# Optimization experiments

Hardware: AMD Instinct MI355X
Metric: run time of the kernel (lower is better)

## Reference

```python
import jax, jax.numpy as jnp
import numpy as np

N_NODES = 50000
NEG_SLOPE = 0.2  # PyG GATConv default
EPS = 1e-16      # PyG softmax denominator epsilon


def _gat_conv(x, edge_index, W, att_src, att_dst, bias):
    """Single-head PyG-style GATConv with self-loops.
    x: [N, F_in], edge_index: [2, E] (row 0 = src/j, row 1 = dst/i).
    """
    n = x.shape[0]
    loop = jnp.arange(n, dtype=edge_index.dtype)
    src = jnp.concatenate([edge_index[0], loop])  # [E+N]
    dst = jnp.concatenate([edge_index[1], loop])  # [E+N]

    h = x @ W                                      # [N, F_out]
    a_src = h @ att_src                            # [N]
    a_dst = h @ att_dst                            # [N]

    e = jax.nn.leaky_relu(a_src[src] + a_dst[dst], NEG_SLOPE)  # [E+N]
    # segment softmax over incoming edges of each dst node
    m = jax.ops.segment_max(e, dst, num_segments=n)
    m = jnp.where(jnp.isfinite(m), m, 0.0)
    e = jnp.exp(e - m[dst])
    s = jax.ops.segment_sum(e, dst, num_segments=n)
    alpha = e / (s[dst] + EPS)                     # [E+N]

    out = jax.ops.segment_sum(alpha[:, None] * h[src], dst, num_segments=n)
    return out + bias


def setup_inputs() -> dict:
    key = jax.random.key(0)
    ks = jax.random.split(key, 10)
    d_in, d_hid, d_emb = 128, 64, 64
    n_edges = 800000
    x = jax.random.normal(ks[0], (N_NODES, d_in), dtype=jnp.float32)
    edge_index = jax.random.randint(ks[1], (2, n_edges), 0, N_NODES, dtype=jnp.int64)
    def glorot(k, shape):
        lim = float(np.sqrt(6.0 / sum(shape)))
        return jax.random.uniform(k, shape, jnp.float32, -lim, lim)
    return {
        "x": x,
        "edge_index": edge_index,
        "W1": glorot(ks[2], (d_in, d_hid)),
        "att_src1": glorot(ks[3], (d_hid,)),
        "att_dst1": glorot(ks[4], (d_hid,)),
        "b1": jnp.zeros((d_hid,), jnp.float32),
        "W2": glorot(ks[5], (d_hid, d_emb)),
        "att_src2": glorot(ks[6], (d_emb,)),
        "att_dst2": glorot(ks[7], (d_emb,)),
        "b2": jnp.zeros((d_emb,), jnp.float32),
    }


def reference(x, edge_index, W1, att_src1, att_dst1, b1, W2, att_src2, att_dst2, b2):
    x1 = jax.nn.relu(_gat_conv(x, edge_index, W1, att_src1, att_dst1, b1))
    # dropout is identity in eval mode
    x2 = _gat_conv(x1, edge_index, W2, att_src2, att_dst2, b2)
    return x2
```

## Files before the change

### kernel.cpp

```cpp
#include <hip/hip_runtime.h>
#include <hip/hip_bf16.h>

#define F_OUT 64
#define NEG_SLOPE 0.2f
#define SOFT_EPS 1e-16f
#define BW 256
#define CH 8192
#define TH 512
#define TH3 512

typedef short short8 __attribute__((ext_vector_type(8)));
typedef float floatx4 __attribute__((ext_vector_type(4)));
typedef unsigned short ushort4v __attribute__((ext_vector_type(4)));
typedef unsigned short ushort8v __attribute__((ext_vector_type(8)));

__device__ __forceinline__ unsigned short f2bf_bits(float v) {
    __hip_bfloat16 hb = __float2bfloat16(v);
    return *(unsigned short*)&hb;
}
__device__ __forceinline__ float bf_bits2f(unsigned short u) {
    __hip_bfloat16 hb = *(__hip_bfloat16*)&u;
    return __bfloat162float(hb);
}
__device__ __forceinline__ float read_any(const void* src, int off, int bf) {
    return bf ? __bfloat162float(((const __hip_bfloat16*)src)[off])
              : ((const float*)src)[off];
}
__device__ __forceinline__ int get_idx(const void* ei, int i64, long long pos) {
    return i64 ? (int)((const long long*)ei)[pos] : ((const int*)ei)[pos];
}

__device__ __forceinline__ void detect_local(const unsigned* wbits, const unsigned* ebits,
                                             int* sm_bf, int* sm_i64) {
    if (threadIdx.x < 64) {
        unsigned w = wbits[threadIdx.x];
        unsigned e = (w >> 7) & 0xFFu;
        unsigned long long mb = __ballot(e >= 0x60u && e <= 0x7Eu);
        unsigned long long mz = __ballot(ebits[2 * threadIdx.x + 1] == 0u);
        if (threadIdx.x == 0) { *sm_bf = (__popcll(mb) > 32); *sm_i64 = (__popcll(mz) > 32); }
    }
    __syncthreads();
}

__global__ void count_prep(const void* __restrict__ ei, int* __restrict__ table,
                           const void* w1, const void* as1, const void* ad1, const void* b1,
                           const void* w2, const void* as2, const void* ad2, const void* b2,
                           unsigned short* __restrict__ wt1, unsigned short* __restrict__ wt2,
                           float* __restrict__ vecs, int* __restrict__ flags,
                           int E, int total, int NB, int nchunks, int n1, int n2, int K1) {
    __shared__ int cnt[1024];
    __shared__ int s_bf, s_i64;
    detect_local((const unsigned*)w1, (const unsigned*)ei, &s_bf, &s_i64);
    int bf = s_bf, i64 = s_i64;
    int g = blockIdx.x, tid = threadIdx.x;
    if (g == 0 && tid == 0) { flags[0] = bf; flags[1] = i64; }

    if (g < nchunks) {
        for (int k = tid; k < NB; k += TH) cnt[k] = 0;
        __syncthreads();
        int base = g * CH;
        int lim = base + CH < total ? base + CH : total;
        for (int t = base + tid; t < lim; t += TH) {
            int i = t < E ? get_idx(ei, i64, (long long)E + t) : t - E;
            atomicAdd(&cnt[i >> 8], 1);
        }
        __syncthreads();
        for (int k = tid; k < NB; k += TH) table[k * nchunks + g] = cnt[k];
    } else {
        int wtotal = n1 + n2 + 384;
        for (int t = tid; t < wtotal; t += TH) {
            if (t < n1) {
                int n = t / K1, k = t - n * K1;
                wt1[t] = f2bf_bits(read_any(w1, k * F_OUT + n, bf));
            } else if (t < n1 + n2) {
                int u = t - n1;
                int n = u >> 6, k = u & 63;
                wt2[u] = f2bf_bits(read_any(w2, k * F_OUT + n, bf));
            } else {
                int u = t - n1 - n2;
                const void* srcp[6] = {as1, ad1, b1, as2, ad2, b2};
                vecs[u] = read_any(srcp[u >> 6], u & 63, bf);
            }
        }
    }
}

template <int K, int WAVES>
__device__ __forceinline__ void gemm_body(int blk, int tid,
                          const void* __restrict__ xv, const unsigned short* __restrict__ Wt,
                          const float* __restrict__ att_s, const float* __restrict__ att_d,
                          unsigned short* __restrict__ h, float* __restrict__ a_s,
                          float* __restrict__ a_d, int N, int bf) {
    int lane = tid & 63;
    int m0 = (blk * WAVES + (tid >> 6)) * 16;
    if (m0 >= N) return;
    int c = lane & 15, quad = lane >> 4;
    int arow = m0 + c;
    if (arow >= N) arow = N - 1;

    floatx4 acc0 = {0.f, 0.f, 0.f, 0.f};
    floatx4 acc1 = acc0, acc2 = acc0, acc3 = acc0;

    for (int kc = 0; kc < K; kc += 32) {
        int ka = kc + quad * 8;
        short8 a;
        if (bf) {
            a = *(const short8*)((const unsigned short*)xv + (size_t)arow * K + ka);
        } else {
            const float* xp = (const float*)xv + (size_t)arow * K + ka;
#pragma unroll
            for (int j = 0; j < 8; ++j) a[j] = (short)f2bf_bits(xp[j]);
        }
        short8 b0 = *(const short8*)(Wt + (size_t)(c)      * K + ka);
        short8 b1 = *(const short8*)(Wt + (size_t)(16 + c) * K + ka);
        short8 b2 = *(const short8*)(Wt + (size_t)(32 + c) * K + ka);
        short8 b3 = *(const short8*)(Wt + (size_t)(48 + c) * K + ka);
        acc0 = __builtin_amdgcn_mfma_f32_16x16x32_bf16(a, b0, acc0, 0, 0, 0);
        acc1 = __builtin_amdgcn_mfma_f32_16x16x32_bf16(a, b1, acc1, 0, 0, 0);
        acc2 = __builtin_amdgcn_mfma_f32_16x16x32_bf16(a, b2, acc2, 0, 0, 0);
        acc3 = __builtin_amdgcn_mfma_f32_16x16x32_bf16(a, b3, acc3, 0, 0, 0);
    }

    float as0 = att_s[c],      as1 = att_s[16 + c], as2 = att_s[32 + c], as3 = att_s[48 + c];
    float ad0 = att_d[c],      ad1 = att_d[16 + c], ad2 = att_d[32 + c], ad3 = att_d[48 + c];
#pragma unroll
    for (int reg = 0; reg < 4; ++reg) {
        int row = m0 + quad * 4 + reg;
        float vs = acc0[reg] * as0 + acc1[reg] * as1 + acc2[reg] * as2 + acc3[reg] * as3;
        float vd = acc0[reg] * ad0 + acc1[reg] * ad1 + acc2[reg] * ad2 + acc3[reg] * ad3;
#pragma unroll
        for (int off = 1; off < 16; off <<= 1) {
            vs += __shfl_xor(vs, off);
            vd += __shfl_xor(vd, off);
        }
        if (row < N) {
            if (c == 0) { a_s[row] = vs; a_d[row] = vd; }
            unsigned short* hr = h + (size_t)row * F_OUT + c;
            hr[0]  = f2bf_bits(acc0[reg]);
            hr[16] = f2bf_bits(acc1[reg]);
            hr[32] = f2bf_bits(acc2[reg]);
            hr[48] = f2bf_bits(acc3[reg]);
        }
    }
}

__global__ void __launch_bounds__(TH)
scatter_gemm1(const void* __restrict__ ei, const int* __restrict__ table,
              unsigned* __restrict__ staged, int* __restrict__ segbeg,
              int* __restrict__ row_ptr, const void* __restrict__ xv,
              const unsigned short* __restrict__ Wt,
              const float* __restrict__ att_s, const float* __restrict__ att_d,
              unsigned short* __restrict__ h, float* __restrict__ a_s,
              float* __restrict__ a_d, const unsigned* __restrict__ wbits,
              int E, int total, int NB, int nchunks, int N) {
    __shared__ int s_bf, s_i64;
    detect_local(wbits, (const unsigned*)ei, &s_bf, &s_i64);
    int tid = threadIdx.x;
    if ((int)blockIdx.x >= nchunks) {
        gemm_body<128, 8>(blockIdx.x - nchunks, tid, xv, Wt, att_s, att_d,
                          h, a_s, a_d, N, s_bf);
        return;
    }
    __shared__ int s_scan[TH];
    __shared__ int s_cur[1024];
    int g = blockIdx.x;
    int i64 = s_i64;
    int b0 = 0;
    if (tid < NB) {
        const int* row = table + (size_t)tid * nchunks;
        int rsum = 0, rpart = 0;
        for (int c2 = 0; c2 < nchunks; ++c2) {
            int v = row[c2];
            rsum += v;
            rpart += (c2 < g) ? v : 0;
        }
        b0 = rsum;
        s_cur[tid] = rpart;
    }
    s_scan[tid] = (tid < NB) ? b0 : 0;
    __syncthreads();
    for (int off = 1; off < TH; off <<= 1) {
        int v = (tid >= off) ? s_scan[tid - off] : 0;
        __syncthreads();
        s_scan[tid] += v;
        __syncthreads();
    }
    if (tid < NB) {
        int excl = s_scan[tid] - b0;
        s_cur[tid] = excl + s_cur[tid];
        if (g == 0) segbeg[tid] = excl;
    }
    if (g == 0 && tid == 0) { segbeg[NB] = total; row_ptr[N] = total; }
    __syncthreads();
    int base = g * CH;
    int lim = base + CH < total ? base + CH : total;
    for (int t = base + tid; t < lim; t += TH) {
        int i = t < E ? get_idx(ei, i64, (long long)E + t) : t - E;
        int j = t < E ? get_idx(ei, i64, t) : t - E;
        int pos = atomicAdd(&s_cur[i >> 8], 1);
        staged[pos] = ((unsigned)(i & 255) << 24) | (unsigned)j;
    }
}

__global__ void __launch_bounds__(TH3)
bucket_csr(const unsigned* __restrict__ staged, const int* __restrict__ segbeg,
           int* __restrict__ row_ptr, int* __restrict__ eidx, int N) {
    __shared__ int ldeg[BW];
    __shared__ int lcur[BW];
    __shared__ int wtot[4];
    int b = blockIdx.x;
    int t = threadIdx.x;
    int seg_beg = segbeg[b];
    int seg_end = segbeg[b + 1];
    if (t < BW) ldeg[t] = 0;
    __syncthreads();
    for (int p = seg_beg + t; p < seg_end; p += TH3)
        atomicAdd(&ldeg[staged[p] >> 24], 1);
    __syncthreads();
    int lane = t & 63, w = t >> 6;
    int d = 0, v = 0;
    if (t < BW) {
        d = ldeg[t];
        v = d;
#pragma unroll
        for (int off = 1; off < 64; off <<= 1) {
            int u = __shfl_up(v, off);
            if (lane >= off) v += u;
        }
        if (lane == 63) wtot[w] = v;
    }
    __syncthreads();
    if (t < BW) {
        int woff = 0;
        for (int k = 0; k < w; ++k) woff += wtot[k];
        int excl = v - d + woff;
        int node = b * BW + t;
        if (node < N) row_ptr[node] = seg_beg + excl;
        lcur[t] = excl;
    }
    __syncthreads();
    for (int p = seg_beg + t; p < seg_end; p += TH3) {
        unsigned pk = staged[p];
        int pos = atomicAdd(&lcur[pk >> 24], 1);
        eidx[seg_beg + pos] = (int)(pk & 0xFFFFFFu);
    }
}

__device__ __forceinline__ void gather_node8(int i, int grp, int c8,
                                             const int* __restrict__ row_ptr,
                                             const int* __restrict__ eidx,
                                             const float* __restrict__ a_s,
                                             const float* __restrict__ a_d,
                                             const unsigned short* __restrict__ h,
                                             float* se_out, float acc[8]) {
    int beg = row_ptr[i];
    int end = row_ptr[i + 1];
    int len = end - beg;
    float ad = a_d[i];
    int gb = beg + ((len * grp) >> 3);
    int ge = beg + ((len * (grp + 1)) >> 3);
    float se = 0.f;
#pragma unroll
    for (int k = 0; k < 8; ++k) acc[k] = 0.f;

    int p = gb;
    for (; p + 1 < ge; p += 2) {
        int j0 = eidx[p];
        int j1 = eidx[p + 1];
        ushort8v hv0 = *(const ushort8v*)(h + (((size_t)j0) << 6) + (c8 << 3));
        ushort8v hv1 = *(const ushort8v*)(h + (((size_t)j1) << 6) + (c8 << 3));
        float e0 = a_s[j0] + ad;
        float e1 = a_s[j1] + ad;
        float w0 = __expf(fmaxf(e0, NEG_SLOPE * e0));
        float w1 = __expf(fmaxf(e1, NEG_SLOPE * e1));
        se += w0 + w1;
#pragma unroll
        for (int k = 0; k < 8; ++k)
            acc[k] += w0 * bf_bits2f(hv0[k]) + w1 * bf_bits2f(hv1[k]);
    }
    if (p < ge) {
        int j0 = eidx[p];
        ushort8v hv0 = *(const ushort8v*)(h + (((size_t)j0) << 6) + (c8 << 3));
        float e0 = a_s[j0] + ad;
        float w0 = __expf(fmaxf(e0, NEG_SLOPE * e0));
        se += w0;
#pragma unroll
        for (int k = 0; k < 8; ++k) acc[k] += w0 * bf_bits2f(hv0[k]);
    }

#pragma unroll
    for (int off = 8; off < 64; off <<= 1) {
        se += __shfl_xor(se, off);
#pragma unroll
        for (int k = 0; k < 8; ++k) acc[k] += __shfl_xor(acc[k], off);
    }
    *se_out = se;
}

#define XST 72
__global__ void __launch_bounds__(1024)
gather1_gemm2(const int* __restrict__ row_ptr, const int* __restrict__ eidx,
              const float* __restrict__ a_s, const float* __restrict__ a_d,
              const unsigned short* __restrict__ h, const float* __restrict__ bias,
              const unsigned short* __restrict__ Wt2,
              const float* __restrict__ att_s2, const float* __restrict__ att_d2,
              unsigned short* __restrict__ h2, float* __restrict__ a_s2,
              float* __restrict__ a_d2, int N) {
    __shared__ unsigned short x1t[16 * XST];
    int tid = threadIdx.x;
    int lane = tid & 63;
    int wv = tid >> 6;
    int grp = lane >> 3, c8 = lane & 7;
    int i = blockIdx.x * 16 + wv;

    if (i < N) {
        float se, acc[8];
        gather_node8(i, grp, c8, row_ptr, eidx, a_s, a_d, h, &se, acc);
        if (grp == 0) {
            int col = c8 << 3;
            float inv = 1.f / (se + SOFT_EPS);
            ushort8v ov;
#pragma unroll
            for (int k = 0; k < 8; ++k) {
                float v = acc[k] * inv + bias[col + k];
                ov[k] = f2bf_bits(v > 0.f ? v : 0.f);
            }
            *(ushort8v*)(x1t + wv * XST + col) = ov;
        }
    } else if (grp == 0) {
        *(ushort8v*)(x1t + wv * XST + (c8 << 3)) = (ushort8v){0, 0, 0, 0, 0, 0, 0, 0};
    }
    __syncthreads();

    if (wv == 0) {
        int quad = lane >> 4, c = lane & 15;
        int m0 = blockIdx.x * 16;
        floatx4 acc0 = {0.f, 0.f, 0.f, 0.f};
        floatx4 acc1 = acc0, acc2 = acc0, acc3 = acc0;
#pragma unroll
        for (int kc = 0; kc < 64; kc += 32) {
            int ka = kc + quad * 8;
            short8 a = *(const short8*)(x1t + c * XST + ka);
            short8 b0 = *(const short8*)(Wt2 + (size_t)(c)      * 64 + ka);
            short8 b1 = *(const short8*)(Wt2 + (size_t)(16 + c) * 64 + ka);
            short8 b2 = *(const short8*)(Wt2 + (size_t)(32 + c) * 64 + ka);
            short8 b3 = *(const short8*)(Wt2 + (size_t)(48 + c) * 64 + ka);
            acc0 = __builtin_amdgcn_mfma_f32_16x16x32_bf16(a, b0, acc0, 0, 0, 0);
            acc1 = __builtin_amdgcn_mfma_f32_16x16x32_bf16(a, b1, acc1, 0, 0, 0);
            acc2 = __builtin_amdgcn_mfma_f32_16x16x32_bf16(a, b2, acc2, 0, 0, 0);
            acc3 = __builtin_amdgcn_mfma_f32_16x16x32_bf16(a, b3, acc3, 0, 0, 0);
        }
        float as0 = att_s2[c],      as1 = att_s2[16 + c], as2 = att_s2[32 + c], as3 = att_s2[48 + c];
        float ad0 = att_d2[c],      ad1 = att_d2[16 + c], ad2 = att_d2[32 + c], ad3 = att_d2[48 + c];
#pragma unroll
        for (int reg = 0; reg < 4; ++reg) {
            int row = m0 + quad * 4 + reg;
            float vs = acc0[reg] * as0 + acc1[reg] * as1 + acc2[reg] * as2 + acc3[reg] * as3;
            float vd = acc0[reg] * ad0 + acc1[reg] * ad1 + acc2[reg] * ad2 + acc3[reg] * ad3;
#pragma unroll
            for (int off = 1; off < 16; off <<= 1) {
                vs += __shfl_xor(vs, off);
                vd += __shfl_xor(vd, off);
            }
            if (row < N) {
                if (c == 0) { a_s2[row] = vs; a_d2[row] = vd; }
                unsigned short* hr = h2 + (size_t)row * F_OUT + c;
                hr[0]  = f2bf_bits(acc0[reg]);
                hr[16] = f2bf_bits(acc1[reg]);
                hr[32] = f2bf_bits(acc2[reg]);
                hr[48] = f2bf_bits(acc3[reg]);
            }
        }
    }
}

__global__ void __launch_bounds__(256)
node_gather_out(const int* __restrict__ row_ptr, const int* __restrict__ eidx,
                const float* __restrict__ a_s, const float* __restrict__ a_d,
                const unsigned short* __restrict__ h, const float* __restrict__ bias,
                void* __restrict__ out, int N, const int* __restrict__ flags) {
    int lane = threadIdx.x & 63;
    int i = blockIdx.x * 4 + (threadIdx.x >> 6);
    if (i >= N) return;
    int grp = lane >> 3, c8 = lane & 7;
    float se, acc[8];
    gather_node8(i, grp, c8, row_ptr, eidx, a_s, a_d, h, &se, acc);
    if (grp == 0) {
        int col = c8 << 3;
        float inv = 1.f / (se + SOFT_EPS);
        float v[8];
#pragma unroll
        for (int k = 0; k < 8; ++k) v[k] = acc[k] * inv + bias[col + k];
        size_t o = (size_t)i * F_OUT + col;
        if (flags[0]) {
            ushort8v ov;
#pragma unroll
            for (int k = 0; k < 8; ++k) ov[k] = f2bf_bits(v[k]);
            *(ushort8v*)((unsigned short*)out + o) = ov;
        } else {
            floatx4 o0 = {v[0], v[1], v[2], v[3]};
            floatx4 o1 = {v[4], v[5], v[6], v[7]};
            *(floatx4*)((float*)out + o) = o0;
            *(floatx4*)((float*)out + o + 4) = o1;
        }
    }
}

extern "C" void kernel_launch(void* const* d_in, const int* in_sizes, int n_in,
                              void* d_out, int out_size, void* d_ws, size_t ws_size,
                              hipStream_t stream) {
    const void* x   = d_in[0];
    const void* ei  = d_in[1];
    const void* W1  = d_in[2];
    const void* as1 = d_in[3];
    const void* ad1 = d_in[4];
    const void* b1  = d_in[5];
    const void* W2  = d_in[6];
    const void* as2 = d_in[7];
    const void* ad2 = d_in[8];
    const void* b2  = d_in[9];

    int E  = in_sizes[1] / 2;
    int n1 = in_sizes[2];
    int n2 = in_sizes[6];
    int K1 = n1 / F_OUT;
    int N  = in_sizes[0] / K1;
    int total = E + N;
    int NB = (N + BW - 1) / BW;
    int nchunks = (total + CH - 1) / CH;
    int M = NB * nchunks;

    size_t nf = (size_t)N * F_OUT;
    char* wsb = (char*)d_ws;
    unsigned short* h   = (unsigned short*)wsb;
    unsigned short* h2  = h + nf;
    unsigned short* wt1 = h2 + nf;
    unsigned short* wt2 = wt1 + n1;
    float* a_s  = (float*)(wt2 + n2 + ((n1 + n2) & 1));
    float* a_d  = a_s + N;
    float* a_s2 = a_d + N;
    float* a_d2 = a_s2 + N;
    float* vecs = a_d2 + N;
    float* cAs1 = vecs,       *cAd1 = vecs + 64,  *cB1 = vecs + 128;
    float* cAs2 = vecs + 192, *cAd2 = vecs + 256, *cB2 = vecs + 320;
    int* flags    = (int*)(vecs + 384);
    int* row_ptr  = flags + 8;
    int* eidx     = row_ptr + N + 1;
    unsigned* staged = (unsigned*)(eidx + total);
    int* table    = (int*)(staged + total);
    int* segbeg   = table + M;

    int blkG1 = (N + 127) / 128;
    int blkFuse = (N + 15) / 16;
    int blkNode = (N + 3) / 4;

    count_prep<<<nchunks + 1, TH, 0, stream>>>(ei, table, W1, as1, ad1, b1,
                                               W2, as2, ad2, b2, wt1, wt2, vecs, flags,
                                               E, total, NB, nchunks, n1, n2, K1);
    scatter_gemm1<<<nchunks + blkG1, TH, 0, stream>>>(ei, table, staged, segbeg, row_ptr,
                                                      x, wt1, cAs1, cAd1, h, a_s, a_d,
                                                      (const unsigned*)W1,
                                                      E, total, NB, nchunks, N);
    bucket_csr<<<NB, TH3, 0, stream>>>(staged, segbeg, row_ptr, eidx, N);
    gather1_gemm2<<<blkFuse, 1024, 0, stream>>>(row_ptr, eidx, a_s, a_d, h, cB1,
                                                wt2, cAs2, cAd2, h2, a_s2, a_d2, N);
    node_gather_out<<<blkNode, 256, 0, stream>>>(row_ptr, eidx, a_s2, a_d2, h2, cB2,
                                                 d_out, N, flags);
}
```

Measured before the change: 188.7 us.

## Fold layer-2 attention vectors into W2 and split layer-2 GEMM across four waves

```diff
diff --git a/kernel.cpp b/kernel.cpp
--- a/kernel.cpp
+++ b/kernel.cpp
@@ -11,7 +11,6 @@
 
 typedef short short8 __attribute__((ext_vector_type(8)));
 typedef float floatx4 __attribute__((ext_vector_type(4)));
-typedef unsigned short ushort4v __attribute__((ext_vector_type(4)));
 typedef unsigned short ushort8v __attribute__((ext_vector_type(8)));
 
 __device__ __forceinline__ unsigned short f2bf_bits(float v) {
@@ -46,7 +45,8 @@
                            const void* w1, const void* as1, const void* ad1, const void* b1,
                            const void* w2, const void* as2, const void* ad2, const void* b2,
                            unsigned short* __restrict__ wt1, unsigned short* __restrict__ wt2,
-                           float* __restrict__ vecs, int* __restrict__ flags,
+                           float* __restrict__ vecs, float* __restrict__ waS2,
+                           float* __restrict__ waD2, int* __restrict__ flags,
                            int E, int total, int NB, int nchunks, int n1, int n2, int K1) {
     __shared__ int cnt[1024];
     __shared__ int s_bf, s_i64;
@@ -82,6 +82,14 @@
                 vecs[u] = read_any(srcp[u >> 6], u & 63, bf);
             }
         }
+        for (int t = tid; t < 128; t += TH) {
+            int k = t & 63;
+            const void* av = (t < 64) ? as2 : ad2;
+            float s = 0.f;
+            for (int n = 0; n < 64; ++n)
+                s += read_any(w2, k * 64 + n, bf) * read_any(av, n, bf);
+            (t < 64 ? waS2 : waD2)[k] = s;
+        }
     }
 }
 
@@ -108,8 +116,13 @@
             a = *(const short8*)((const unsigned short*)xv + (size_t)arow * K + ka);
         } else {
             const float* xp = (const float*)xv + (size_t)arow * K + ka;
-#pragma unroll
-            for (int j = 0; j < 8; ++j) a[j] = (short)f2bf_bits(xp[j]);
+            floatx4 f0 = *(const floatx4*)xp;
+            floatx4 f1 = *(const floatx4*)(xp + 4);
+#pragma unroll
+            for (int j = 0; j < 4; ++j) {
+                a[j]     = (short)f2bf_bits(f0[j]);
+                a[4 + j] = (short)f2bf_bits(f1[j]);
+            }
         }
         short8 b0 = *(const short8*)(Wt + (size_t)(c)      * K + ka);
         short8 b1 = *(const short8*)(Wt + (size_t)(16 + c) * K + ka);
@@ -298,12 +311,12 @@
 }
 
 #define XST 72
-__global__ void __launch_bounds__(1024)
+__global__ void __launch_bounds__(1024, 2)
 gather1_gemm2(const int* __restrict__ row_ptr, const int* __restrict__ eidx,
               const float* __restrict__ a_s, const float* __restrict__ a_d,
               const unsigned short* __restrict__ h, const float* __restrict__ bias,
               const unsigned short* __restrict__ Wt2,
-              const float* __restrict__ att_s2, const float* __restrict__ att_d2,
+              const float* __restrict__ waS2, const float* __restrict__ waD2,
               unsigned short* __restrict__ h2, float* __restrict__ a_s2,
               float* __restrict__ a_d2, int N) {
     __shared__ unsigned short x1t[16 * XST];
@@ -316,15 +329,34 @@
     if (i < N) {
         float se, acc[8];
         gather_node8(i, grp, c8, row_ptr, eidx, a_s, a_d, h, &se, acc);
+        int col = c8 << 3;
+        float inv = 1.f / (se + SOFT_EPS);
+        floatx4 ws0 = *(const floatx4*)(waS2 + col);
+        floatx4 ws1 = *(const floatx4*)(waS2 + col + 4);
+        floatx4 wd0 = *(const floatx4*)(waD2 + col);
+        floatx4 wd1 = *(const floatx4*)(waD2 + col + 4);
+        float v[8];
+        float ps = 0.f, pd = 0.f;
+#pragma unroll
+        for (int k = 0; k < 8; ++k) {
+            float x = acc[k] * inv + bias[col + k];
+            x = x > 0.f ? x : 0.f;
+            v[k] = x;
+            float fs = (k < 4) ? ws0[k] : ws1[k - 4];
+            float fd = (k < 4) ? wd0[k] : wd1[k - 4];
+            ps += x * fs;
+            pd += x * fd;
+        }
+#pragma unroll
+        for (int off = 1; off < 8; off <<= 1) {
+            ps += __shfl_xor(ps, off);
+            pd += __shfl_xor(pd, off);
+        }
+        if (lane == 0) { a_s2[i] = ps; a_d2[i] = pd; }
         if (grp == 0) {
-            int col = c8 << 3;
-            float inv = 1.f / (se + SOFT_EPS);
             ushort8v ov;
 #pragma unroll
-            for (int k = 0; k < 8; ++k) {
-                float v = acc[k] * inv + bias[col + k];
-                ov[k] = f2bf_bits(v > 0.f ? v : 0.f);
-            }
+            for (int k = 0; k < 8; ++k) ov[k] = f2bf_bits(v[k]);
             *(ushort8v*)(x1t + wv * XST + col) = ov;
         }
     } else if (grp == 0) {
@@ -332,49 +364,26 @@
     }
     __syncthreads();
 
-    if (wv == 0) {
+    if (wv < 4) {
         int quad = lane >> 4, c = lane & 15;
         int m0 = blockIdx.x * 16;
-        floatx4 acc0 = {0.f, 0.f, 0.f, 0.f};
-        floatx4 acc1 = acc0, acc2 = acc0, acc3 = acc0;
+        floatx4 g0 = {0.f, 0.f, 0.f, 0.f};
 #pragma unroll
         for (int kc = 0; kc < 64; kc += 32) {
             int ka = kc + quad * 8;
             short8 a = *(const short8*)(x1t + c * XST + ka);
-            short8 b0 = *(const short8*)(Wt2 + (size_t)(c)      * 64 + ka);
-            short8 b1 = *(const short8*)(Wt2 + (size_t)(16 + c) * 64 + ka);
-            short8 b2 = *(const short8*)(Wt2 + (size_t)(32 + c) * 64 + ka);
-            short8 b3 = *(const short8*)(Wt2 + (size_t)(48 + c) * 64 + ka);
-            acc0 = __builtin_amdgcn_mfma_f32_16x16x32_bf16(a, b0, acc0, 0, 0, 0);
-            acc1 = __builtin_amdgcn_mfma_f32_16x16x32_bf16(a, b1, acc1, 0, 0, 0);
-            acc2 = __builtin_amdgcn_mfma_f32_16x16x32_bf16(a, b2, acc2, 0, 0, 0);
-            acc3 = __builtin_amdgcn_mfma_f32_16x16x32_bf16(a, b3, acc3, 0, 0, 0);
-        }
-        float as0 = att_s2[c],      as1 = att_s2[16 + c], as2 = att_s2[32 + c], as3 = att_s2[48 + c];
-        float ad0 = att_d2[c],      ad1 = att_d2[16 + c], ad2 = att_d2[32 + c], ad3 = att_d2[48 + c];
+            short8 b = *(const short8*)(Wt2 + (size_t)(wv * 16 + c) * 64 + ka);
+            g0 = __builtin_amdgcn_mfma_f32_16x16x32_bf16(a, b, g0, 0, 0, 0);
+        }
 #pragma unroll
         for (int reg = 0; reg < 4; ++reg) {
             int row = m0 + quad * 4 + reg;
-            float vs = acc0[reg] * as0 + acc1[reg] * as1 + acc2[reg] * as2 + acc3[reg] * as3;
-            float vd = acc0[reg] * ad0 + acc1[reg] * ad1 + acc2[reg] * ad2 + acc3[reg] * ad3;
-#pragma unroll
-            for (int off = 1; off < 16; off <<= 1) {
-                vs += __shfl_xor(vs, off);
-                vd += __shfl_xor(vd, off);
-            }
-            if (row < N) {
-                if (c == 0) { a_s2[row] = vs; a_d2[row] = vd; }
-                unsigned short* hr = h2 + (size_t)row * F_OUT + c;
-                hr[0]  = f2bf_bits(acc0[reg]);
-                hr[16] = f2bf_bits(acc1[reg]);
-                hr[32] = f2bf_bits(acc2[reg]);
-                hr[48] = f2bf_bits(acc3[reg]);
-            }
-        }
-    }
-}
-
-__global__ void __launch_bounds__(256)
+            if (row < N) h2[(size_t)row * F_OUT + wv * 16 + c] = f2bf_bits(g0[reg]);
+        }
+    }
+}
+
+__global__ void __launch_bounds__(256, 8)
 node_gather_out(const int* __restrict__ row_ptr, const int* __restrict__ eidx,
                 const float* __restrict__ a_s, const float* __restrict__ a_d,
                 const unsigned short* __restrict__ h, const float* __restrict__ bias,
@@ -443,7 +452,9 @@
     float* vecs = a_d2 + N;
     float* cAs1 = vecs,       *cAd1 = vecs + 64,  *cB1 = vecs + 128;
     float* cAs2 = vecs + 192, *cAd2 = vecs + 256, *cB2 = vecs + 320;
-    int* flags    = (int*)(vecs + 384);
+    float* waS2 = vecs + 384;
+    float* waD2 = vecs + 448;
+    int* flags    = (int*)(vecs + 512);
     int* row_ptr  = flags + 8;
     int* eidx     = row_ptr + N + 1;
     unsigned* staged = (unsigned*)(eidx + total);
@@ -455,7 +466,8 @@
     int blkNode = (N + 3) / 4;
 
     count_prep<<<nchunks + 1, TH, 0, stream>>>(ei, table, W1, as1, ad1, b1,
-                                               W2, as2, ad2, b2, wt1, wt2, vecs, flags,
+                                               W2, as2, ad2, b2, wt1, wt2, vecs,
+                                               waS2, waD2, flags,
                                                E, total, NB, nchunks, n1, n2, K1);
     scatter_gemm1<<<nchunks + blkG1, TH, 0, stream>>>(ei, table, staged, segbeg, row_ptr,
                                                       x, wt1, cAs1, cAd1, h, a_s, a_d,
@@ -463,7 +475,7 @@
                                                       E, total, NB, nchunks, N);
     bucket_csr<<<NB, TH3, 0, stream>>>(staged, segbeg, row_ptr, eidx, N);
     gather1_gemm2<<<blkFuse, 1024, 0, stream>>>(row_ptr, eidx, a_s, a_d, h, cB1,
-                                                wt2, cAs2, cAd2, h2, a_s2, a_d2, N);
+                                                wt2, waS2, waD2, h2, a_s2, a_d2, N);
     node_gather_out<<<blkNode, 256, 0, stream>>>(row_ptr, eidx, a_s2, a_d2, h2, cB2,
                                                  d_out, N, flags);
 }
```

After: 192.9 us. 2.3% more time.

## Sort nodes by degree within buckets to balance fused gather-GEMM blocks

Applied to the files above, without the earlier changes.

```diff
diff --git a/kernel.cpp b/kernel.cpp
--- a/kernel.cpp
+++ b/kernel.cpp
@@ -5,13 +5,12 @@
 #define NEG_SLOPE 0.2f
 #define SOFT_EPS 1e-16f
 #define BW 256
-#define CH 8192
+#define CH 4096
 #define TH 512
-#define TH3 512
+#define TH3 1024
 
 typedef short short8 __attribute__((ext_vector_type(8)));
 typedef float floatx4 __attribute__((ext_vector_type(4)));
-typedef unsigned short ushort4v __attribute__((ext_vector_type(4)));
 typedef unsigned short ushort8v __attribute__((ext_vector_type(8)));
 
 __device__ __forceinline__ unsigned short f2bf_bits(float v) {
@@ -108,8 +107,13 @@
             a = *(const short8*)((const unsigned short*)xv + (size_t)arow * K + ka);
         } else {
             const float* xp = (const float*)xv + (size_t)arow * K + ka;
-#pragma unroll
-            for (int j = 0; j < 8; ++j) a[j] = (short)f2bf_bits(xp[j]);
+            floatx4 f0 = *(const floatx4*)xp;
+            floatx4 f1 = *(const floatx4*)(xp + 4);
+#pragma unroll
+            for (int j = 0; j < 4; ++j) {
+                a[j]     = (short)f2bf_bits(f0[j]);
+                a[4 + j] = (short)f2bf_bits(f1[j]);
+            }
         }
         short8 b0 = *(const short8*)(Wt + (size_t)(c)      * K + ka);
         short8 b1 = *(const short8*)(Wt + (size_t)(16 + c) * K + ka);
@@ -204,23 +208,29 @@
 
 __global__ void __launch_bounds__(TH3)
 bucket_csr(const unsigned* __restrict__ staged, const int* __restrict__ segbeg,
-           int* __restrict__ row_ptr, int* __restrict__ eidx, int N) {
+           int* __restrict__ row_ptr, int* __restrict__ eidx,
+           int* __restrict__ order, int N) {
     __shared__ int ldeg[BW];
     __shared__ int lcur[BW];
     __shared__ int wtot[4];
+    __shared__ int dcnt[128];
+    __shared__ int dcur[128];
     int b = blockIdx.x;
     int t = threadIdx.x;
     int seg_beg = segbeg[b];
     int seg_end = segbeg[b + 1];
     if (t < BW) ldeg[t] = 0;
+    if (t < 128) dcnt[t] = 0;
     __syncthreads();
     for (int p = seg_beg + t; p < seg_end; p += TH3)
         atomicAdd(&ldeg[staged[p] >> 24], 1);
     __syncthreads();
     int lane = t & 63, w = t >> 6;
-    int d = 0, v = 0;
+    int node = b * BW + t;
+    int d = 0, v = 0, dmin = 0;
     if (t < BW) {
         d = ldeg[t];
+        dmin = d < 127 ? d : 127;
         v = d;
 #pragma unroll
         for (int off = 1; off < 64; off <<= 1) {
@@ -234,11 +244,28 @@
         int woff = 0;
         for (int k = 0; k < w; ++k) woff += wtot[k];
         int excl = v - d + woff;
-        int node = b * BW + t;
-        if (node < N) row_ptr[node] = seg_beg + excl;
+        if (node < N) {
+            row_ptr[node] = seg_beg + excl;
+            atomicAdd(&dcnt[dmin], 1);
+        }
         lcur[t] = excl;
-    }
-    __syncthreads();
+        order[b * BW + t] = -1;
+    }
+    __syncthreads();
+    if (t < 128) dcur[t] = dcnt[t];
+    __syncthreads();
+    for (int off = 1; off < 128; off <<= 1) {
+        int u = (t < 128 && t >= off) ? dcnt[t - off] : 0;
+        __syncthreads();
+        if (t < 128) dcnt[t] += u;
+        __syncthreads();
+    }
+    if (t < 128) dcur[t] = dcnt[t] - dcur[t];
+    __syncthreads();
+    if (t < BW && node < N) {
+        int pos = atomicAdd(&dcur[dmin], 1);
+        order[b * BW + pos] = node;
+    }
     for (int p = seg_beg + t; p < seg_end; p += TH3) {
         unsigned pk = staged[p];
         int pos = atomicAdd(&lcur[pk >> 24], 1);
@@ -300,6 +327,7 @@
 #define XST 72
 __global__ void __launch_bounds__(1024)
 gather1_gemm2(const int* __restrict__ row_ptr, const int* __restrict__ eidx,
+              const int* __restrict__ order,
               const float* __restrict__ a_s, const float* __restrict__ a_d,
               const unsigned short* __restrict__ h, const float* __restrict__ bias,
               const unsigned short* __restrict__ Wt2,
@@ -307,13 +335,15 @@
               unsigned short* __restrict__ h2, float* __restrict__ a_s2,
               float* __restrict__ a_d2, int N) {
     __shared__ unsigned short x1t[16 * XST];
+    __shared__ int nid[16];
     int tid = threadIdx.x;
     int lane = tid & 63;
     int wv = tid >> 6;
     int grp = lane >> 3, c8 = lane & 7;
-    int i = blockIdx.x * 16 + wv;
-
-    if (i < N) {
+    int i = order[blockIdx.x * 16 + wv];
+
+    if ((unsigned)i < (unsigned)N) {
+        if (lane == 0) nid[wv] = i;
         float se, acc[8];
         gather_node8(i, grp, c8, row_ptr, eidx, a_s, a_d, h, &se, acc);
         if (grp == 0) {
@@ -327,14 +357,15 @@
             }
             *(ushort8v*)(x1t + wv * XST + col) = ov;
         }
-    } else if (grp == 0) {
-        *(ushort8v*)(x1t + wv * XST + (c8 << 3)) = (ushort8v){0, 0, 0, 0, 0, 0, 0, 0};
+    } else {
+        if (lane == 0) nid[wv] = -1;
+        if (grp == 0)
+            *(ushort8v*)(x1t + wv * XST + (c8 << 3)) = (ushort8v){0, 0, 0, 0, 0, 0, 0, 0};
     }
     __syncthreads();
 
     if (wv == 0) {
         int quad = lane >> 4, c = lane & 15;
-        int m0 = blockIdx.x * 16;
         floatx4 acc0 = {0.f, 0.f, 0.f, 0.f};
         floatx4 acc1 = acc0, acc2 = acc0, acc3 = acc0;
 #pragma unroll
@@ -354,7 +385,7 @@
         float ad0 = att_d2[c],      ad1 = att_d2[16 + c], ad2 = att_d2[32 + c], ad3 = att_d2[48 + c];
 #pragma unroll
         for (int reg = 0; reg < 4; ++reg) {
-            int row = m0 + quad * 4 + reg;
+            int nd = nid[quad * 4 + reg];
             float vs = acc0[reg] * as0 + acc1[reg] * as1 + acc2[reg] * as2 + acc3[reg] * as3;
             float vd = acc0[reg] * ad0 + acc1[reg] * ad1 + acc2[reg] * ad2 + acc3[reg] * ad3;
 #pragma unroll
@@ -362,9 +393,9 @@
                 vs += __shfl_xor(vs, off);
                 vd += __shfl_xor(vd, off);
             }
-            if (row < N) {
-                if (c == 0) { a_s2[row] = vs; a_d2[row] = vd; }
-                unsigned short* hr = h2 + (size_t)row * F_OUT + c;
+            if ((unsigned)nd < (unsigned)N) {
+                if (c == 0) { a_s2[nd] = vs; a_d2[nd] = vd; }
+                unsigned short* hr = h2 + (size_t)nd * F_OUT + c;
                 hr[0]  = f2bf_bits(acc0[reg]);
                 hr[16] = f2bf_bits(acc1[reg]);
                 hr[32] = f2bf_bits(acc2[reg]);
@@ -449,6 +480,7 @@
     unsigned* staged = (unsigned*)(eidx + total);
     int* table    = (int*)(staged + total);
     int* segbeg   = table + M;
+    int* order    = segbeg + NB + 1;
 
     int blkG1 = (N + 127) / 128;
     int blkFuse = (N + 15) / 16;
@@ -461,8 +493,8 @@
                                                       x, wt1, cAs1, cAd1, h, a_s, a_d,
                                                       (const unsigned*)W1,
                                                       E, total, NB, nchunks, N);
-    bucket_csr<<<NB, TH3, 0, stream>>>(staged, segbeg, row_ptr, eidx, N);
-    gather1_gemm2<<<blkFuse, 1024, 0, stream>>>(row_ptr, eidx, a_s, a_d, h, cB1,
+    bucket_csr<<<NB, TH3, 0, stream>>>(staged, segbeg, row_ptr, eidx, order, N);
+    gather1_gemm2<<<blkFuse, 1024, 0, stream>>>(row_ptr, eidx, order, a_s, a_d, h, cB1,
                                                 wt2, cAs2, cAd2, h2, a_s2, a_d2, N);
     node_gather_out<<<blkNode, 256, 0, stream>>>(row_ptr, eidx, a_s2, a_d2, h2, cB2,
                                                  d_out, N, flags);
```

Result: slower. 199.5 us (+5.7%).

## Process two destination nodes per wave in gather kernels for more memory parallelism

Applied to the files above, without the earlier changes.

```diff
diff --git a/kernel.cpp b/kernel.cpp
--- a/kernel.cpp
+++ b/kernel.cpp
@@ -11,7 +11,6 @@
 
 typedef short short8 __attribute__((ext_vector_type(8)));
 typedef float floatx4 __attribute__((ext_vector_type(4)));
-typedef unsigned short ushort4v __attribute__((ext_vector_type(4)));
 typedef unsigned short ushort8v __attribute__((ext_vector_type(8)));
 
 __device__ __forceinline__ unsigned short f2bf_bits(float v) {
@@ -108,8 +107,13 @@
             a = *(const short8*)((const unsigned short*)xv + (size_t)arow * K + ka);
         } else {
             const float* xp = (const float*)xv + (size_t)arow * K + ka;
-#pragma unroll
-            for (int j = 0; j < 8; ++j) a[j] = (short)f2bf_bits(xp[j]);
+            floatx4 f0 = *(const floatx4*)xp;
+            floatx4 f1 = *(const floatx4*)(xp + 4);
+#pragma unroll
+            for (int j = 0; j < 4; ++j) {
+                a[j]     = (short)f2bf_bits(f0[j]);
+                a[4 + j] = (short)f2bf_bits(f1[j]);
+            }
         }
         short8 b0 = *(const short8*)(Wt + (size_t)(c)      * K + ka);
         short8 b1 = *(const short8*)(Wt + (size_t)(16 + c) * K + ka);
@@ -246,59 +250,79 @@
     }
 }
 
-__device__ __forceinline__ void gather_node8(int i, int grp, int c8,
-                                             const int* __restrict__ row_ptr,
-                                             const int* __restrict__ eidx,
-                                             const float* __restrict__ a_s,
-                                             const float* __restrict__ a_d,
-                                             const unsigned short* __restrict__ h,
-                                             float* se_out, float acc[8]) {
-    int beg = row_ptr[i];
-    int end = row_ptr[i + 1];
-    int len = end - beg;
-    float ad = a_d[i];
-    int gb = beg + ((len * grp) >> 3);
-    int ge = beg + ((len * (grp + 1)) >> 3);
-    float se = 0.f;
-#pragma unroll
-    for (int k = 0; k < 8; ++k) acc[k] = 0.f;
-
-    int p = gb;
-    for (; p + 1 < ge; p += 2) {
-        int j0 = eidx[p];
-        int j1 = eidx[p + 1];
-        ushort8v hv0 = *(const ushort8v*)(h + (((size_t)j0) << 6) + (c8 << 3));
-        ushort8v hv1 = *(const ushort8v*)(h + (((size_t)j1) << 6) + (c8 << 3));
-        float e0 = a_s[j0] + ad;
-        float e1 = a_s[j1] + ad;
-        float w0 = __expf(fmaxf(e0, NEG_SLOPE * e0));
-        float w1 = __expf(fmaxf(e1, NEG_SLOPE * e1));
-        se += w0 + w1;
-#pragma unroll
-        for (int k = 0; k < 8; ++k)
-            acc[k] += w0 * bf_bits2f(hv0[k]) + w1 * bf_bits2f(hv1[k]);
-    }
-    if (p < ge) {
-        int j0 = eidx[p];
-        ushort8v hv0 = *(const ushort8v*)(h + (((size_t)j0) << 6) + (c8 << 3));
-        float e0 = a_s[j0] + ad;
-        float w0 = __expf(fmaxf(e0, NEG_SLOPE * e0));
-        se += w0;
-#pragma unroll
-        for (int k = 0; k < 8; ++k) acc[k] += w0 * bf_bits2f(hv0[k]);
+__device__ __forceinline__ void gather_node8x2(int ia, int ib, int grp, int c8,
+                                               const int* __restrict__ row_ptr,
+                                               const int* __restrict__ eidx,
+                                               const float* __restrict__ a_s,
+                                               const float* __restrict__ a_d,
+                                               const unsigned short* __restrict__ h,
+                                               float* sea_out, float acca[8],
+                                               float* seb_out, float accb[8], int N) {
+    const char* hb8 = (const char*)h;
+    unsigned cofs = (unsigned)(c8 << 4);
+    int bega = row_ptr[ia], enda = row_ptr[ia + 1];
+    int lena = enda - bega;
+    float ada = a_d[ia];
+    int pa = bega + ((lena * grp) >> 3);
+    int gea = bega + ((lena * (grp + 1)) >> 3);
+    int pb = 0, geb = 0;
+    float adb = 0.f;
+    if (ib < N) {
+        int begb = row_ptr[ib], endb = row_ptr[ib + 1];
+        int lenb = endb - begb;
+        adb = a_d[ib];
+        pb = begb + ((lenb * grp) >> 3);
+        geb = begb + ((lenb * (grp + 1)) >> 3);
+    }
+    float sea = 0.f, seb = 0.f;
+#pragma unroll
+    for (int k = 0; k < 8; ++k) { acca[k] = 0.f; accb[k] = 0.f; }
+
+    while (pa < gea || pb < geb) {
+        bool va0 = pa < gea, va1 = pa + 1 < gea;
+        bool vb0 = pb < geb, vb1 = pb + 1 < geb;
+        int ja0 = va0 ? eidx[pa]     : 0;
+        int ja1 = va1 ? eidx[pa + 1] : 0;
+        int jb0 = vb0 ? eidx[pb]     : 0;
+        int jb1 = vb1 ? eidx[pb + 1] : 0;
+        ushort8v ha0 = *(const ushort8v*)(hb8 + (((unsigned)ja0 << 7) + cofs));
+        ushort8v ha1 = *(const ushort8v*)(hb8 + (((unsigned)ja1 << 7) + cofs));
+        ushort8v hb0 = *(const ushort8v*)(hb8 + (((unsigned)jb0 << 7) + cofs));
+        ushort8v hb1 = *(const ushort8v*)(hb8 + (((unsigned)jb1 << 7) + cofs));
+        float ea0 = a_s[ja0] + ada;
+        float ea1 = a_s[ja1] + ada;
+        float eb0 = a_s[jb0] + adb;
+        float eb1 = a_s[jb1] + adb;
+        float wa0 = va0 ? __expf(fmaxf(ea0, NEG_SLOPE * ea0)) : 0.f;
+        float wa1 = va1 ? __expf(fmaxf(ea1, NEG_SLOPE * ea1)) : 0.f;
+        float wb0 = vb0 ? __expf(fmaxf(eb0, NEG_SLOPE * eb0)) : 0.f;
+        float wb1 = vb1 ? __expf(fmaxf(eb1, NEG_SLOPE * eb1)) : 0.f;
+        sea += wa0 + wa1;
+        seb += wb0 + wb1;
+#pragma unroll
+        for (int k = 0; k < 8; ++k) {
+            acca[k] += wa0 * bf_bits2f(ha0[k]) + wa1 * bf_bits2f(ha1[k]);
+            accb[k] += wb0 * bf_bits2f(hb0[k]) + wb1 * bf_bits2f(hb1[k]);
+        }
+        pa += 2; pb += 2;
     }
 
 #pragma unroll
     for (int off = 8; off < 64; off <<= 1) {
-        se += __shfl_xor(se, off);
-#pragma unroll
-        for (int k = 0; k < 8; ++k) acc[k] += __shfl_xor(acc[k], off);
-    }
-    *se_out = se;
+        sea += __shfl_xor(sea, off);
+        seb += __shfl_xor(seb, off);
+#pragma unroll
+        for (int k = 0; k < 8; ++k) {
+            acca[k] += __shfl_xor(acca[k], off);
+            accb[k] += __shfl_xor(accb[k], off);
+        }
+    }
+    *sea_out = sea;
+    *seb_out = seb;
 }
 
 #define XST 72
-__global__ void __launch_bounds__(1024)
+__global__ void __launch_bounds__(512)
 gather1_gemm2(const int* __restrict__ row_ptr, const int* __restrict__ eidx,
               const float* __restrict__ a_s, const float* __restrict__ a_d,
               const unsigned short* __restrict__ h, const float* __restrict__ bias,
@@ -311,24 +335,38 @@
     int lane = tid & 63;
     int wv = tid >> 6;
     int grp = lane >> 3, c8 = lane & 7;
-    int i = blockIdx.x * 16 + wv;
-
-    if (i < N) {
-        float se, acc[8];
-        gather_node8(i, grp, c8, row_ptr, eidx, a_s, a_d, h, &se, acc);
+    int ia = blockIdx.x * 16 + (wv << 1);
+    int ib = ia + 1;
+
+    if (ia < N) {
+        float sea, seb, acca[8], accb[8];
+        gather_node8x2(ia, ib, grp, c8, row_ptr, eidx, a_s, a_d, h,
+                       &sea, acca, &seb, accb, N);
         if (grp == 0) {
             int col = c8 << 3;
-            float inv = 1.f / (se + SOFT_EPS);
+            float inv = 1.f / (sea + SOFT_EPS);
             ushort8v ov;
 #pragma unroll
             for (int k = 0; k < 8; ++k) {
-                float v = acc[k] * inv + bias[col + k];
+                float v = acca[k] * inv + bias[col + k];
                 ov[k] = f2bf_bits(v > 0.f ? v : 0.f);
             }
-            *(ushort8v*)(x1t + wv * XST + col) = ov;
+            *(ushort8v*)(x1t + (wv * 2) * XST + col) = ov;
+            if (ib < N) {
+                inv = 1.f / (seb + SOFT_EPS);
+#pragma unroll
+                for (int k = 0; k < 8; ++k) {
+                    float v = accb[k] * inv + bias[col + k];
+                    ov[k] = f2bf_bits(v > 0.f ? v : 0.f);
+                }
+            } else {
+                ov = (ushort8v){0, 0, 0, 0, 0, 0, 0, 0};
+            }
+            *(ushort8v*)(x1t + (wv * 2 + 1) * XST + col) = ov;
         }
     } else if (grp == 0) {
-        *(ushort8v*)(x1t + wv * XST + (c8 << 3)) = (ushort8v){0, 0, 0, 0, 0, 0, 0, 0};
+        *(ushort8v*)(x1t + (wv * 2)     * XST + (c8 << 3)) = (ushort8v){0, 0, 0, 0, 0, 0, 0, 0};
+        *(ushort8v*)(x1t + (wv * 2 + 1) * XST + (c8 << 3)) = (ushort8v){0, 0, 0, 0, 0, 0, 0, 0};
     }
     __syncthreads();
 
@@ -380,28 +418,39 @@
                 const unsigned short* __restrict__ h, const float* __restrict__ bias,
                 void* __restrict__ out, int N, const int* __restrict__ flags) {
     int lane = threadIdx.x & 63;
-    int i = blockIdx.x * 4 + (threadIdx.x >> 6);
-    if (i >= N) return;
+    int wv = threadIdx.x >> 6;
+    int ia = blockIdx.x * 8 + (wv << 1);
+    int ib = ia + 1;
+    if (ia >= N) return;
     int grp = lane >> 3, c8 = lane & 7;
-    float se, acc[8];
-    gather_node8(i, grp, c8, row_ptr, eidx, a_s, a_d, h, &se, acc);
+    float sea, seb, acca[8], accb[8];
+    gather_node8x2(ia, ib, grp, c8, row_ptr, eidx, a_s, a_d, h,
+                   &sea, acca, &seb, accb, N);
     if (grp == 0) {
         int col = c8 << 3;
-        float inv = 1.f / (se + SOFT_EPS);
-        float v[8];
-#pragma unroll
-        for (int k = 0; k < 8; ++k) v[k] = acc[k] * inv + bias[col + k];
-        size_t o = (size_t)i * F_OUT + col;
-        if (flags[0]) {
-            ushort8v ov;
-#pragma unroll
-            for (int k = 0; k < 8; ++k) ov[k] = f2bf_bits(v[k]);
-            *(ushort8v*)((unsigned short*)out + o) = ov;
-        } else {
-            floatx4 o0 = {v[0], v[1], v[2], v[3]};
-            floatx4 o1 = {v[4], v[5], v[6], v[7]};
-            *(floatx4*)((float*)out + o) = o0;
-            *(floatx4*)((float*)out + o + 4) = o1;
+        int obf = flags[0];
+#pragma unroll
+        for (int nn = 0; nn < 2; ++nn) {
+            int i = nn ? ib : ia;
+            if (i >= N) break;
+            float se = nn ? seb : sea;
+            const float* ac = nn ? accb : acca;
+            float inv = 1.f / (se + SOFT_EPS);
+            float v[8];
+#pragma unroll
+            for (int k = 0; k < 8; ++k) v[k] = ac[k] * inv + bias[col + k];
+            size_t o = (size_t)i * F_OUT + col;
+            if (obf) {
+                ushort8v ov;
+#pragma unroll
+                for (int k = 0; k < 8; ++k) ov[k] = f2bf_bits(v[k]);
+                *(ushort8v*)((unsigned short*)out + o) = ov;
+            } else {
+                floatx4 o0 = {v[0], v[1], v[2], v[3]};
+                floatx4 o1 = {v[4], v[5], v[6], v[7]};
+                *(floatx4*)((float*)out + o) = o0;
+                *(floatx4*)((float*)out + o + 4) = o1;
+            }
         }
     }
 }
@@ -452,7 +501,7 @@
 
     int blkG1 = (N + 127) / 128;
     int blkFuse = (N + 15) / 16;
-    int blkNode = (N + 3) / 4;
+    int blkNode = (N + 7) / 8;
 
     count_prep<<<nchunks + 1, TH, 0, stream>>>(ei, table, W1, as1, ad1, b1,
                                                W2, as2, ad2, b2, wt1, wt2, vecs, flags,
@@ -462,8 +511,8 @@
                                                       (const unsigned*)W1,
                                                       E, total, NB, nchunks, N);
     bucket_csr<<<NB, TH3, 0, stream>>>(staged, segbeg, row_ptr, eidx, N);
-    gather1_gemm2<<<blkFuse, 1024, 0, stream>>>(row_ptr, eidx, a_s, a_d, h, cB1,
-                                                wt2, cAs2, cAd2, h2, a_s2, a_d2, N);
+    gather1_gemm2<<<blkFuse, 512, 0, stream>>>(row_ptr, eidx, a_s, a_d, h, cB1,
+                                               wt2, cAs2, cAd2, h2, a_s2, a_d2, N);
     node_gather_out<<<blkNode, 256, 0, stream>>>(row_ptr, eidx, a_s2, a_d2, h2, cB2,
                                                  d_out, N, flags);
 }
```

Result: faster. 179.8 us (-4.7%).
